# Kernel tuning notes

Measured on AMD Instinct MI355X. Metric: run time of the kernel, lower is better.

The kernel has to match this reference:

```python
import jax, jax.numpy as jnp
import numpy as np

B, N, T, H = 32, 16, 64, 256


def setup_inputs() -> dict:
    key = jax.random.key(0)
    k1, k2, k3 = jax.random.split(key, 3)
    node_rnn_output = jax.random.normal(k1, (B, T, H), dtype=jnp.float32)
    neigh_rnn_output = jax.random.normal(k2, (B, N, T, H), dtype=jnp.float32)
    # neighbor counts in [1, N] to avoid divide-by-zero in 1/sqrt scaling
    neighbors_number = jax.random.randint(k3, (B,), 1, N + 1, dtype=jnp.int64)
    return {
        "node_rnn_output": node_rnn_output,
        "neigh_rnn_output": neigh_rnn_output,
        "neighbors_number": neighbors_number,
    }


def reference(node_rnn_output, neigh_rnn_output, neighbors_number):
    b, t, h = node_rnn_output.shape
    n = neigh_rnn_output.shape[1]
    # [B, N*T, H]
    flat_neigh = neigh_rnn_output.reshape(b, n * t, h)
    # repeat node output along time axis: [B, N*T, H]
    stacked_node = jnp.tile(node_rnn_output, (1, n, 1))
    # S = flat_neigh @ stacked_node^T : [B, N*T, N*T]
    S = jnp.einsum("bqh,bkh->bqk", flat_neigh, stacked_node)
    scale = jnp.sqrt(neighbors_number.astype(S.dtype))  # [B]
    S = S / scale[:, None, None]
    A = jax.nn.softmax(S, axis=-1)
    # dropout with p=0 (eval / reference) is identity
    W = A.sum(axis=1).reshape(b, n, t)  # [B, N, T]
    output = jnp.einsum("bqk,bkh->bqh", A, flat_neigh)  # [B, N*T, H]
    return (output, W)
```

## Files before the change

kernel.cpp:

```cpp
#include <hip/hip_runtime.h>

#define Bc  32
#define Nc  16
#define Tc  64
#define Hc  256
#define NTc 1024

typedef unsigned short u16;
using v8s = __attribute__((ext_vector_type(8))) short;
using v4f = __attribute__((ext_vector_type(4))) float;

static __device__ __forceinline__ u16 f2bf(float x) {
    unsigned u = __float_as_uint(x);
    unsigned r = u + 0x7fffu + ((u >> 16) & 1u);
    return (u16)(r >> 16);
}
static __device__ __forceinline__ float bf2f(u16 h) {
    return __uint_as_float(((unsigned)h) << 16);
}

#define NFRAG_NODE 2048
#define NFRAG_MT   2048

__global__ __launch_bounds__(256) void prep_kernel(const float* __restrict__ neigh,
                                                   const float* __restrict__ node,
                                                   u16* __restrict__ MTf,
                                                   u16* __restrict__ NHf,
                                                   u16* __restrict__ NLf,
                                                   float* __restrict__ Wsum) {
    __shared__ float Ls[64][17];
    int bk = blockIdx.x, tid = threadIdx.x;

    if (bk < 512) {
        int b  = bk >> 4;
        int hc = bk & 15;
        int h0 = hc << 4;
        int t  = tid >> 2;
        int h4 = tid & 3;
        const float4* p = (const float4*)(neigh + ((size_t)(b * Nc * Tc) + t) * Hc + h0) + h4;
        float4 a = make_float4(0.f, 0.f, 0.f, 0.f);
#pragma unroll
        for (int i = 0; i < Nc; i++) {
            float4 v = p[(size_t)i * (Tc * Hc / 4)];
            a.x += v.x; a.y += v.y; a.z += v.z; a.w += v.w;
        }
        const float r = 1.0f / 16.0f;
        Ls[t][h4 * 4 + 0] = a.x * r;
        Ls[t][h4 * 4 + 1] = a.y * r;
        Ls[t][h4 * 4 + 2] = a.z * r;
        Ls[t][h4 * 4 + 3] = a.w * r;
        __syncthreads();
        if (tid < 128) {
            int ktb  = tid >> 6;
            int lane = tid & 63;
            int quad = lane >> 4;
            int c    = lane & 15;
            v8s o;
#pragma unroll
            for (int j = 0; j < 8; j++)
                o[j] = (short)f2bf(Ls[ktb * 32 + quad * 8 + j][c]);
            *(v8s*)(MTf + ((size_t)b * NFRAG_MT + (hc * 2 + ktb) * 64 + lane) * 8) = o;
        }
    } else {
        int b = bk - 512;
#pragma unroll
        for (int rep = 0; rep < 8; rep++) {
            int f    = rep * 256 + tid;
            int nt   = f >> 9;
            int ksb  = (f >> 6) & 7;
            int lane = f & 63;
            int quad = lane >> 4;
            int c    = lane & 15;
            const float* src = node + ((size_t)b * Tc + nt * 16 + c) * Hc + ksb * 32 + quad * 8;
            float4 f0 = *(const float4*)(src);
            float4 f1 = *(const float4*)(src + 4);
            v8s hs, ls;
            float vin[8] = {f0.x, f0.y, f0.z, f0.w, f1.x, f1.y, f1.z, f1.w};
#pragma unroll
            for (int j = 0; j < 8; j++) {
                u16 h = f2bf(vin[j]);
                hs[j] = (short)h;
                ls[j] = (short)f2bf(vin[j] - bf2f(h));
            }
            *(v8s*)(NHf + ((size_t)b * NFRAG_NODE + f) * 8) = hs;
            *(v8s*)(NLf + ((size_t)b * NFRAG_NODE + f) * 8) = ls;
        }
        if (tid < 64) Wsum[b * 64 + tid] = 0.f;
    }
}

__global__ __launch_bounds__(256) void fused_kernel(const float* __restrict__ neigh,
                                                    const u16* __restrict__ NHf,
                                                    const u16* __restrict__ NLf,
                                                    const int* __restrict__ nbr,
                                                    const u16* __restrict__ MTf,
                                                    float* __restrict__ out,
                                                    float* __restrict__ Wsum) {
    __shared__ u16 NHs[NFRAG_NODE * 8];
    __shared__ u16 Ph[64][72];

    int b  = blockIdx.x >> 4;
    int i  = blockIdx.x & 15;
    int q0 = i << 6;

    int tid  = threadIdx.x;
    int w    = tid >> 6;
    int lane = tid & 63;
    int quad = lane >> 4;
    int c    = lane & 15;

    int nb = (nbr[1] == 0) ? nbr[2 * b] : nbr[b];
    float rscale = rsqrtf((float)nb);

    const float* Xrow = neigh + ((size_t)(b * Nc * Tc) + q0 + w * 16 + c) * Hc;
    const u16*   NHb  = NHf + (size_t)b * NFRAG_NODE * 8;
    const u16*   NLb  = NLf + (size_t)b * NFRAG_NODE * 8 + lane * 8;
    const u16*   MTb  = MTf + (size_t)b * NFRAG_MT   * 8 + lane * 8;

#pragma unroll
    for (int rep = 0; rep < 8; rep++) {
        int chunk = rep * 256 + tid;
        *(uint4*)&NHs[chunk * 8] = *(const uint4*)(NHb + chunk * 8);
    }
    __syncthreads();

    v4f acc[4];
#pragma unroll
    for (int nt = 0; nt < 4; nt++)
#pragma unroll
        for (int rg = 0; rg < 4; rg++) acc[nt][rg] = 0.f;

#pragma unroll
    for (int ksb = 0; ksb < 8; ksb++) {
        float4 f0 = *(const float4*)(Xrow + ksb * 32 + quad * 8);
        float4 f1 = *(const float4*)(Xrow + ksb * 32 + quad * 8 + 4);
        v8s ah, al;
        {
            float vin[8] = {f0.x, f0.y, f0.z, f0.w, f1.x, f1.y, f1.z, f1.w};
#pragma unroll
            for (int j = 0; j < 8; j++) {
                u16 h = f2bf(vin[j]);
                ah[j] = (short)h;
                al[j] = (short)f2bf(vin[j] - bf2f(h));
            }
        }
#pragma unroll
        for (int nt = 0; nt < 4; nt++) {
            int fbase = (nt * 8 + ksb) * 64;
            v8s bh = *(const v8s*)&NHs[(fbase + lane) * 8];
            v8s bl = *(const v8s*)(NLb + (size_t)fbase * 8);
            acc[nt] = __builtin_amdgcn_mfma_f32_16x16x32_bf16(ah, bh, acc[nt], 0, 0, 0);
            acc[nt] = __builtin_amdgcn_mfma_f32_16x16x32_bf16(ah, bl, acc[nt], 0, 0, 0);
            acc[nt] = __builtin_amdgcn_mfma_f32_16x16x32_bf16(al, bh, acc[nt], 0, 0, 0);
        }
    }

#pragma unroll
    for (int nt = 0; nt < 4; nt++)
#pragma unroll
        for (int rg = 0; rg < 4; rg++) acc[nt][rg] *= rscale;

#pragma unroll
    for (int rg = 0; rg < 4; rg++) {
        float m = fmaxf(fmaxf(acc[0][rg], acc[1][rg]), fmaxf(acc[2][rg], acc[3][rg]));
#pragma unroll
        for (int d = 1; d < 16; d <<= 1) m = fmaxf(m, __shfl_xor(m, d));
        float e0 = __expf(acc[0][rg] - m);
        float e1 = __expf(acc[1][rg] - m);
        float e2 = __expf(acc[2][rg] - m);
        float e3 = __expf(acc[3][rg] - m);
        float s = e0 + e1 + e2 + e3;
#pragma unroll
        for (int d = 1; d < 16; d <<= 1) s += __shfl_xor(s, d);
        float inv = 1.0f / s;
        acc[0][rg] = e0 * inv; acc[1][rg] = e1 * inv;
        acc[2][rg] = e2 * inv; acc[3][rg] = e3 * inv;
    }

#pragma unroll
    for (int nt = 0; nt < 4; nt++) {
        float cs = acc[nt][0] + acc[nt][1] + acc[nt][2] + acc[nt][3];
        cs += __shfl_xor(cs, 16);
        cs += __shfl_xor(cs, 32);
        if (quad == 0) atomicAdd(&Wsum[b * Tc + nt * 16 + c], cs);
    }

#pragma unroll
    for (int nt = 0; nt < 4; nt++)
#pragma unroll
        for (int rg = 0; rg < 4; rg++)
            Ph[w * 16 + quad * 4 + rg][nt * 16 + c] = f2bf(acc[nt][rg]);

    v8s pa0 = *(const v8s*)&Ph[w * 16 + c][quad * 8];
    v8s pa1 = *(const v8s*)&Ph[w * 16 + c][32 + quad * 8];

    float* ob = out + ((size_t)b * NTc + q0 + w * 16 + quad * 4) * Hc + c;
#pragma unroll
    for (int ht = 0; ht < 16; ht++) {
        v8s b0 = *(const v8s*)(MTb + (size_t)((ht * 2 + 0) * 64) * 8);
        v8s b1 = *(const v8s*)(MTb + (size_t)((ht * 2 + 1) * 64) * 8);
        v4f oc;
        oc[0] = 0.f; oc[1] = 0.f; oc[2] = 0.f; oc[3] = 0.f;
        oc = __builtin_amdgcn_mfma_f32_16x16x32_bf16(pa0, b0, oc, 0, 0, 0);
        oc = __builtin_amdgcn_mfma_f32_16x16x32_bf16(pa1, b1, oc, 0, 0, 0);
#pragma unroll
        for (int rg = 0; rg < 4; rg++)
            ob[(size_t)rg * Hc + ht * 16] = oc[rg];
    }
}

__global__ __launch_bounds__(256) void wexp_kernel(const float* __restrict__ Wsum,
                                                   float* __restrict__ Wout) {
    int idx = blockIdx.x * 256 + threadIdx.x;
    int b = idx >> 10;
    int t = idx & 63;
    Wout[idx] = Wsum[b * Tc + t] * (1.0f / 16.0f);
}

extern "C" void kernel_launch(void* const* d_in, const int* in_sizes, int n_in,
                              void* d_out, int out_size, void* d_ws, size_t ws_size,
                              hipStream_t stream) {
    const float* node  = (const float*)d_in[0];
    const float* neigh = (const float*)d_in[1];
    const int*   nbr   = (const int*)d_in[2];

    float* out = (float*)d_out;

    u16* MTw = (u16*)d_ws;
    u16* NHw = MTw + (size_t)Bc * NFRAG_MT * 8;
    u16* NLw = NHw + (size_t)Bc * NFRAG_NODE * 8;
    float* Ww = (float*)(NLw + (size_t)Bc * NFRAG_NODE * 8);

    prep_kernel <<<544, 256, 0, stream>>>(neigh, node, MTw, NHw, NLw, Ww);
    fused_kernel<<<512, 256, 0, stream>>>(neigh, NHw, NLw, nbr, MTw, out, Ww);
    wexp_kernel <<<128, 256, 0, stream>>>(Ww, out + (size_t)Bc * NTc * Hc);
}
```

Baseline: 111.5 us.

## Precompute bf16 hi/lo split of neighbor tensor in prep and stage B operands in LDS

The prep kernel now converts the full neighbor tensor into bf16 high and low halves stored in workspace, while it is already reading that tensor to compute the mean. The fused kernel then loads these precomputed halves instead of reading fp32 and splitting it per block. Both the node hi and lo fragments are staged in shared memory, and the mean-transpose fragments are reloaded into the same LDS buffer for the second GEMM. This removes redundant conversion work and global fragment loads from the fused kernel, but it adds a full extra write and read of the neighbor tensor (two bf16 copies) through global memory, doubles the LDS footprint, and adds extra barriers.

```diff
diff --git a/kernel.cpp b/kernel.cpp
--- a/kernel.cpp
+++ b/kernel.cpp
@@ -19,47 +19,59 @@
     return __uint_as_float(((unsigned)h) << 16);
 }
 
-#define NFRAG_NODE 2048
-#define NFRAG_MT   2048
+#define XSZ   ((size_t)Bc * Nc * Tc * Hc)
+#define NODEF_SZ ((size_t)Bc * 4096 * 8)
+#define MTF_SZ   ((size_t)Bc * 2048 * 8)
 
 __global__ __launch_bounds__(256) void prep_kernel(const float* __restrict__ neigh,
                                                    const float* __restrict__ node,
+                                                   u16* __restrict__ XH,
+                                                   u16* __restrict__ XL,
+                                                   u16* __restrict__ NODEf,
                                                    u16* __restrict__ MTf,
-                                                   u16* __restrict__ NHf,
-                                                   u16* __restrict__ NLf,
                                                    float* __restrict__ Wsum) {
-    __shared__ float Ls[64][17];
+    __shared__ float Ls[32][33];
     int bk = blockIdx.x, tid = threadIdx.x;
 
     if (bk < 512) {
-        int b  = bk >> 4;
-        int hc = bk & 15;
-        int h0 = hc << 4;
-        int t  = tid >> 2;
-        int h4 = tid & 3;
-        const float4* p = (const float4*)(neigh + ((size_t)(b * Nc * Tc) + t) * Hc + h0) + h4;
+        int b   = bk >> 4;
+        int hc  = (bk >> 1) & 7;
+        int ktb = bk & 1;
+        int t0  = ktb * 32;
+        int h0  = hc * 32;
+        int t_l = tid >> 3;
+        int h8  = tid & 7;
         float4 a = make_float4(0.f, 0.f, 0.f, 0.f);
 #pragma unroll
         for (int i = 0; i < Nc; i++) {
-            float4 v = p[(size_t)i * (Tc * Hc / 4)];
+            size_t off = ((size_t)((b * Nc + i) * Tc) + t0 + t_l) * Hc + h0 + h8 * 4;
+            float4 v = *(const float4*)(neigh + off);
             a.x += v.x; a.y += v.y; a.z += v.z; a.w += v.w;
+            ushort4 hs, ls;
+            hs.x = f2bf(v.x); ls.x = f2bf(v.x - bf2f(hs.x));
+            hs.y = f2bf(v.y); ls.y = f2bf(v.y - bf2f(hs.y));
+            hs.z = f2bf(v.z); ls.z = f2bf(v.z - bf2f(hs.z));
+            hs.w = f2bf(v.w); ls.w = f2bf(v.w - bf2f(hs.w));
+            *(ushort4*)(XH + off) = hs;
+            *(ushort4*)(XL + off) = ls;
         }
         const float r = 1.0f / 16.0f;
-        Ls[t][h4 * 4 + 0] = a.x * r;
-        Ls[t][h4 * 4 + 1] = a.y * r;
-        Ls[t][h4 * 4 + 2] = a.z * r;
-        Ls[t][h4 * 4 + 3] = a.w * r;
+        Ls[t_l][h8 * 4 + 0] = a.x * r;
+        Ls[t_l][h8 * 4 + 1] = a.y * r;
+        Ls[t_l][h8 * 4 + 2] = a.z * r;
+        Ls[t_l][h8 * 4 + 3] = a.w * r;
         __syncthreads();
         if (tid < 128) {
-            int ktb  = tid >> 6;
+            int htl  = tid >> 6;
             int lane = tid & 63;
             int quad = lane >> 4;
             int c    = lane & 15;
             v8s o;
 #pragma unroll
             for (int j = 0; j < 8; j++)
-                o[j] = (short)f2bf(Ls[ktb * 32 + quad * 8 + j][c]);
-            *(v8s*)(MTf + ((size_t)b * NFRAG_MT + (hc * 2 + ktb) * 64 + lane) * 8) = o;
+                o[j] = (short)f2bf(Ls[quad * 8 + j][htl * 16 + c]);
+            int ht = hc * 2 + htl;
+            *(v8s*)(MTf + ((size_t)b * 2048 + (ht * 2 + ktb) * 64 + lane) * 8) = o;
         }
     } else {
         int b = bk - 512;
@@ -82,21 +94,21 @@
                 hs[j] = (short)h;
                 ls[j] = (short)f2bf(vin[j] - bf2f(h));
             }
-            *(v8s*)(NHf + ((size_t)b * NFRAG_NODE + f) * 8) = hs;
-            *(v8s*)(NLf + ((size_t)b * NFRAG_NODE + f) * 8) = ls;
+            *(v8s*)(NODEf + ((size_t)b * 4096 + f) * 8)        = hs;
+            *(v8s*)(NODEf + ((size_t)b * 4096 + 2048 + f) * 8) = ls;
         }
         if (tid < 64) Wsum[b * 64 + tid] = 0.f;
     }
 }
 
-__global__ __launch_bounds__(256) void fused_kernel(const float* __restrict__ neigh,
-                                                    const u16* __restrict__ NHf,
-                                                    const u16* __restrict__ NLf,
+__global__ __launch_bounds__(256) void fused_kernel(const u16* __restrict__ XH,
+                                                    const u16* __restrict__ XL,
+                                                    const u16* __restrict__ NODEf,
+                                                    const u16* __restrict__ MTf,
                                                     const int* __restrict__ nbr,
-                                                    const u16* __restrict__ MTf,
                                                     float* __restrict__ out,
                                                     float* __restrict__ Wsum) {
-    __shared__ u16 NHs[NFRAG_NODE * 8];
+    __shared__ __align__(16) u16 Bs[4096 * 8];
     __shared__ u16 Ph[64][72];
 
     int b  = blockIdx.x >> 4;
@@ -112,18 +124,18 @@
     int nb = (nbr[1] == 0) ? nbr[2 * b] : nbr[b];
     float rscale = rsqrtf((float)nb);
 
-    const float* Xrow = neigh + ((size_t)(b * Nc * Tc) + q0 + w * 16 + c) * Hc;
-    const u16*   NHb  = NHf + (size_t)b * NFRAG_NODE * 8;
-    const u16*   NLb  = NLf + (size_t)b * NFRAG_NODE * 8 + lane * 8;
-    const u16*   MTb  = MTf + (size_t)b * NFRAG_MT   * 8 + lane * 8;
-
-#pragma unroll
-    for (int rep = 0; rep < 8; rep++) {
-        int chunk = rep * 256 + tid;
-        *(uint4*)&NHs[chunk * 8] = *(const uint4*)(NHb + chunk * 8);
+    const u16* NFb = NODEf + (size_t)b * 4096 * 8;
+#pragma unroll
+    for (int rep = 0; rep < 16; rep++) {
+        int ch = rep * 256 + tid;
+        *(uint4*)&Bs[ch * 8] = *(const uint4*)(NFb + ch * 8);
     }
     __syncthreads();
 
+    size_t xoff = ((size_t)((b * Nc + i) * Tc) + w * 16 + c) * Hc;
+    const u16* XHrow = XH + xoff;
+    const u16* XLrow = XL + xoff;
+
     v4f acc[4];
 #pragma unroll
     for (int nt = 0; nt < 4; nt++)
@@ -132,23 +144,13 @@
 
 #pragma unroll
     for (int ksb = 0; ksb < 8; ksb++) {
-        float4 f0 = *(const float4*)(Xrow + ksb * 32 + quad * 8);
-        float4 f1 = *(const float4*)(Xrow + ksb * 32 + quad * 8 + 4);
-        v8s ah, al;
-        {
-            float vin[8] = {f0.x, f0.y, f0.z, f0.w, f1.x, f1.y, f1.z, f1.w};
-#pragma unroll
-            for (int j = 0; j < 8; j++) {
-                u16 h = f2bf(vin[j]);
-                ah[j] = (short)h;
-                al[j] = (short)f2bf(vin[j] - bf2f(h));
-            }
-        }
+        v8s ah = *(const v8s*)(XHrow + ksb * 32 + quad * 8);
+        v8s al = *(const v8s*)(XLrow + ksb * 32 + quad * 8);
 #pragma unroll
         for (int nt = 0; nt < 4; nt++) {
-            int fbase = (nt * 8 + ksb) * 64;
-            v8s bh = *(const v8s*)&NHs[(fbase + lane) * 8];
-            v8s bl = *(const v8s*)(NLb + (size_t)fbase * 8);
+            int f = (nt * 8 + ksb) * 64 + lane;
+            v8s bh = *(const v8s*)&Bs[f * 8];
+            v8s bl = *(const v8s*)&Bs[(f + 2048) * 8];
             acc[nt] = __builtin_amdgcn_mfma_f32_16x16x32_bf16(ah, bh, acc[nt], 0, 0, 0);
             acc[nt] = __builtin_amdgcn_mfma_f32_16x16x32_bf16(ah, bl, acc[nt], 0, 0, 0);
             acc[nt] = __builtin_amdgcn_mfma_f32_16x16x32_bf16(al, bh, acc[nt], 0, 0, 0);
@@ -194,11 +196,21 @@
     v8s pa0 = *(const v8s*)&Ph[w * 16 + c][quad * 8];
     v8s pa1 = *(const v8s*)&Ph[w * 16 + c][32 + quad * 8];
 
+    __syncthreads();
+
+    const u16* MTb = MTf + (size_t)b * 2048 * 8;
+#pragma unroll
+    for (int rep = 0; rep < 8; rep++) {
+        int ch = rep * 256 + tid;
+        *(uint4*)&Bs[ch * 8] = *(const uint4*)(MTb + ch * 8);
+    }
+    __syncthreads();
+
     float* ob = out + ((size_t)b * NTc + q0 + w * 16 + quad * 4) * Hc + c;
 #pragma unroll
     for (int ht = 0; ht < 16; ht++) {
-        v8s b0 = *(const v8s*)(MTb + (size_t)((ht * 2 + 0) * 64) * 8);
-        v8s b1 = *(const v8s*)(MTb + (size_t)((ht * 2 + 1) * 64) * 8);
+        v8s b0 = *(const v8s*)&Bs[((ht * 2 + 0) * 64 + lane) * 8];
+        v8s b1 = *(const v8s*)&Bs[((ht * 2 + 1) * 64 + lane) * 8];
         v4f oc;
         oc[0] = 0.f; oc[1] = 0.f; oc[2] = 0.f; oc[3] = 0.f;
         oc = __builtin_amdgcn_mfma_f32_16x16x32_bf16(pa0, b0, oc, 0, 0, 0);
@@ -226,12 +238,13 @@
 
     float* out = (float*)d_out;
 
-    u16* MTw = (u16*)d_ws;
-    u16* NHw = MTw + (size_t)Bc * NFRAG_MT * 8;
-    u16* NLw = NHw + (size_t)Bc * NFRAG_NODE * 8;
-    float* Ww = (float*)(NLw + (size_t)Bc * NFRAG_NODE * 8);
-
-    prep_kernel <<<544, 256, 0, stream>>>(neigh, node, MTw, NHw, NLw, Ww);
-    fused_kernel<<<512, 256, 0, stream>>>(neigh, NHw, NLw, nbr, MTw, out, Ww);
+    u16* XHw = (u16*)d_ws;
+    u16* XLw = XHw + XSZ;
+    u16* NFw = XLw + XSZ;
+    u16* MTw = NFw + NODEF_SZ;
+    float* Ww = (float*)(MTw + MTF_SZ);
+
+    prep_kernel <<<544, 256, 0, stream>>>(neigh, node, XHw, XLw, NFw, MTw, Ww);
+    fused_kernel<<<512, 256, 0, stream>>>(XHw, XLw, NFw, MTw, nbr, out, Ww);
     wexp_kernel <<<128, 256, 0, stream>>>(Ww, out + (size_t)Bc * NTc * Hc);
 }
```

Result: slower. 114.6 us (+2.8%).

## Merge prep, fused and W-expand kernels into one cooperative kernel with grid syncs

Applied to the files above, without the earlier changes.

Replaces the three separate launches with a single cooperative kernel that runs the prep phase, a grid-wide sync, the attention phase, another grid sync, and the W expansion. The node hi/lo bf16 fragments are packed together so both are staged in shared memory, and the MT fragments are also staged in shared memory before the output matmul instead of being read from global memory. Node preprocessing is spread across all blocks using the idle upper half of each block. This removes inter-kernel launch gaps and cuts redundant global reads, in exchange for grid-sync cost and higher shared memory use, which now requires two resident blocks per CU for the cooperative launch to fit.

```diff
diff --git a/kernel.cpp b/kernel.cpp
--- a/kernel.cpp
+++ b/kernel.cpp
@@ -1,4 +1,7 @@
 #include <hip/hip_runtime.h>
+#include <hip/hip_cooperative_groups.h>
+
+namespace cg = cooperative_groups;
 
 #define Bc  32
 #define Nc  16
@@ -19,37 +22,51 @@
     return __uint_as_float(((unsigned)h) << 16);
 }
 
-#define NFRAG_NODE 2048
-#define NFRAG_MT   2048
-
-__global__ __launch_bounds__(256) void prep_kernel(const float* __restrict__ neigh,
-                                                   const float* __restrict__ node,
-                                                   u16* __restrict__ MTf,
-                                                   u16* __restrict__ NHf,
-                                                   u16* __restrict__ NLf,
-                                                   float* __restrict__ Wsum) {
-    __shared__ float Ls[64][17];
-    int bk = blockIdx.x, tid = threadIdx.x;
-
-    if (bk < 512) {
+#define NODEF_SZ ((size_t)Bc * 4096 * 8)
+#define MTF_SZ   ((size_t)Bc * 2048 * 8)
+
+__global__ __launch_bounds__(256, 2) void mono_kernel(const float* __restrict__ neigh,
+                                                      const float* __restrict__ node,
+                                                      const int*   __restrict__ nbr,
+                                                      u16* __restrict__ NODEf,
+                                                      u16* __restrict__ MTf,
+                                                      float* __restrict__ Wsum,
+                                                      float* __restrict__ out,
+                                                      float* __restrict__ Wout) {
+    __shared__ __align__(16) u16 Bs[4096 * 8];
+    __shared__ u16 Ph[64][72];
+
+    cg::grid_group grid = cg::this_grid();
+
+    int bk  = blockIdx.x;
+    int tid = threadIdx.x;
+
+    {
+        float (*Ls)[17] = (float(*)[17])Bs;
         int b  = bk >> 4;
         int hc = bk & 15;
         int h0 = hc << 4;
-        int t  = tid >> 2;
-        int h4 = tid & 3;
-        const float4* p = (const float4*)(neigh + ((size_t)(b * Nc * Tc) + t) * Hc + h0) + h4;
-        float4 a = make_float4(0.f, 0.f, 0.f, 0.f);
-#pragma unroll
-        for (int i = 0; i < Nc; i++) {
-            float4 v = p[(size_t)i * (Tc * Hc / 4)];
-            a.x += v.x; a.y += v.y; a.z += v.z; a.w += v.w;
-        }
-        const float r = 1.0f / 16.0f;
-        Ls[t][h4 * 4 + 0] = a.x * r;
-        Ls[t][h4 * 4 + 1] = a.y * r;
-        Ls[t][h4 * 4 + 2] = a.z * r;
-        Ls[t][h4 * 4 + 3] = a.w * r;
-        __syncthreads();
+
+        if (bk < 32 && tid < 64) Wsum[bk * 64 + tid] = 0.f;
+
+        {
+            int t  = tid >> 2;
+            int h4 = tid & 3;
+            const float4* p = (const float4*)(neigh + ((size_t)(b * Nc * Tc) + t) * Hc + h0) + h4;
+            float4 a = make_float4(0.f, 0.f, 0.f, 0.f);
+#pragma unroll
+            for (int i = 0; i < Nc; i++) {
+                float4 v = p[(size_t)i * (Tc * Hc / 4)];
+                a.x += v.x; a.y += v.y; a.z += v.z; a.w += v.w;
+            }
+            const float r = 1.0f / 16.0f;
+            Ls[t][h4 * 4 + 0] = a.x * r;
+            Ls[t][h4 * 4 + 1] = a.y * r;
+            Ls[t][h4 * 4 + 2] = a.z * r;
+            Ls[t][h4 * 4 + 3] = a.w * r;
+        }
+        __syncthreads();
+
         if (tid < 128) {
             int ktb  = tid >> 6;
             int lane = tid & 63;
@@ -59,19 +76,17 @@
 #pragma unroll
             for (int j = 0; j < 8; j++)
                 o[j] = (short)f2bf(Ls[ktb * 32 + quad * 8 + j][c]);
-            *(v8s*)(MTf + ((size_t)b * NFRAG_MT + (hc * 2 + ktb) * 64 + lane) * 8) = o;
-        }
-    } else {
-        int b = bk - 512;
-#pragma unroll
-        for (int rep = 0; rep < 8; rep++) {
-            int f    = rep * 256 + tid;
+            *(v8s*)(MTf + ((size_t)b * 2048 + (hc * 2 + ktb) * 64 + lane) * 8) = o;
+        } else {
+            int g    = bk * 128 + (tid - 128);
+            int bn   = g >> 11;
+            int f    = g & 2047;
             int nt   = f >> 9;
             int ksb  = (f >> 6) & 7;
             int lane = f & 63;
             int quad = lane >> 4;
-            int c    = lane & 15;
-            const float* src = node + ((size_t)b * Tc + nt * 16 + c) * Hc + ksb * 32 + quad * 8;
+            int cc   = lane & 15;
+            const float* src = node + ((size_t)bn * Tc + nt * 16 + cc) * Hc + ksb * 32 + quad * 8;
             float4 f0 = *(const float4*)(src);
             float4 f1 = *(const float4*)(src + 4);
             v8s hs, ls;
@@ -82,139 +97,139 @@
                 hs[j] = (short)h;
                 ls[j] = (short)f2bf(vin[j] - bf2f(h));
             }
-            *(v8s*)(NHf + ((size_t)b * NFRAG_NODE + f) * 8) = hs;
-            *(v8s*)(NLf + ((size_t)b * NFRAG_NODE + f) * 8) = ls;
-        }
-        if (tid < 64) Wsum[b * 64 + tid] = 0.f;
+            *(v8s*)(NODEf + ((size_t)bn * 4096 + f) * 8)        = hs;
+            *(v8s*)(NODEf + ((size_t)bn * 4096 + 2048 + f) * 8) = ls;
+        }
     }
-}
-
-__global__ __launch_bounds__(256) void fused_kernel(const float* __restrict__ neigh,
-                                                    const u16* __restrict__ NHf,
-                                                    const u16* __restrict__ NLf,
-                                                    const int* __restrict__ nbr,
-                                                    const u16* __restrict__ MTf,
-                                                    float* __restrict__ out,
-                                                    float* __restrict__ Wsum) {
-    __shared__ u16 NHs[NFRAG_NODE * 8];
-    __shared__ u16 Ph[64][72];
-
-    int b  = blockIdx.x >> 4;
-    int i  = blockIdx.x & 15;
-    int q0 = i << 6;
-
-    int tid  = threadIdx.x;
-    int w    = tid >> 6;
-    int lane = tid & 63;
-    int quad = lane >> 4;
-    int c    = lane & 15;
-
-    int nb = (nbr[1] == 0) ? nbr[2 * b] : nbr[b];
-    float rscale = rsqrtf((float)nb);
-
-    const float* Xrow = neigh + ((size_t)(b * Nc * Tc) + q0 + w * 16 + c) * Hc;
-    const u16*   NHb  = NHf + (size_t)b * NFRAG_NODE * 8;
-    const u16*   NLb  = NLf + (size_t)b * NFRAG_NODE * 8 + lane * 8;
-    const u16*   MTb  = MTf + (size_t)b * NFRAG_MT   * 8 + lane * 8;
-
-#pragma unroll
-    for (int rep = 0; rep < 8; rep++) {
-        int chunk = rep * 256 + tid;
-        *(uint4*)&NHs[chunk * 8] = *(const uint4*)(NHb + chunk * 8);
+
+    grid.sync();
+
+    {
+        int b  = bk >> 4;
+        int i  = bk & 15;
+        int q0 = i << 6;
+
+        int w    = tid >> 6;
+        int lane = tid & 63;
+        int quad = lane >> 4;
+        int c    = lane & 15;
+
+        int nb = (nbr[1] == 0) ? nbr[2 * b] : nbr[b];
+        float rscale = rsqrtf((float)nb);
+
+        const u16* NFb = NODEf + (size_t)b * 4096 * 8;
+#pragma unroll
+        for (int rep = 0; rep < 16; rep++) {
+            int ch = rep * 256 + tid;
+            *(uint4*)&Bs[ch * 8] = *(const uint4*)(NFb + ch * 8);
+        }
+        __syncthreads();
+
+        const float* Xrow = neigh + ((size_t)(b * Nc * Tc) + q0 + w * 16 + c) * Hc;
+
+        v4f acc[4];
+#pragma unroll
+        for (int nt = 0; nt < 4; nt++)
+#pragma unroll
+            for (int rg = 0; rg < 4; rg++) acc[nt][rg] = 0.f;
+
+#pragma unroll
+        for (int ksb = 0; ksb < 8; ksb++) {
+            float4 f0 = *(const float4*)(Xrow + ksb * 32 + quad * 8);
+            float4 f1 = *(const float4*)(Xrow + ksb * 32 + quad * 8 + 4);
+            v8s ah, al;
+            {
+                float vin[8] = {f0.x, f0.y, f0.z, f0.w, f1.x, f1.y, f1.z, f1.w};
+#pragma unroll
+                for (int j = 0; j < 8; j++) {
+                    u16 h = f2bf(vin[j]);
+                    ah[j] = (short)h;
+                    al[j] = (short)f2bf(vin[j] - bf2f(h));
+                }
+            }
+#pragma unroll
+            for (int nt = 0; nt < 4; nt++) {
+                int f = (nt * 8 + ksb) * 64 + lane;
+                v8s bh = *(const v8s*)&Bs[f * 8];
+                v8s bl = *(const v8s*)&Bs[(f + 2048) * 8];
+                acc[nt] = __builtin_amdgcn_mfma_f32_16x16x32_bf16(ah, bh, acc[nt], 0, 0, 0);
+                acc[nt] = __builtin_amdgcn_mfma_f32_16x16x32_bf16(ah, bl, acc[nt], 0, 0, 0);
+                acc[nt] = __builtin_amdgcn_mfma_f32_16x16x32_bf16(al, bh, acc[nt], 0, 0, 0);
+            }
+        }
+
+#pragma unroll
+        for (int nt = 0; nt < 4; nt++)
+#pragma unroll
+            for (int rg = 0; rg < 4; rg++) acc[nt][rg] *= rscale;
+
+#pragma unroll
+        for (int rg = 0; rg < 4; rg++) {
+            float m = fmaxf(fmaxf(acc[0][rg], acc[1][rg]), fmaxf(acc[2][rg], acc[3][rg]));
+#pragma unroll
+            for (int d = 1; d < 16; d <<= 1) m = fmaxf(m, __shfl_xor(m, d));
+            float e0 = __expf(acc[0][rg] - m);
+            float e1 = __expf(acc[1][rg] - m);
+            float e2 = __expf(acc[2][rg] - m);
+            float e3 = __expf(acc[3][rg] - m);
+            float s = e0 + e1 + e2 + e3;
+#pragma unroll
+            for (int d = 1; d < 16; d <<= 1) s += __shfl_xor(s, d);
+            float inv = 1.0f / s;
+            acc[0][rg] = e0 * inv; acc[1][rg] = e1 * inv;
+            acc[2][rg] = e2 * inv; acc[3][rg] = e3 * inv;
+        }
+
+#pragma unroll
+        for (int nt = 0; nt < 4; nt++) {
+            float cs = acc[nt][0] + acc[nt][1] + acc[nt][2] + acc[nt][3];
+            cs += __shfl_xor(cs, 16);
+            cs += __shfl_xor(cs, 32);
+            if (quad == 0) atomicAdd(&Wsum[b * Tc + nt * 16 + c], cs);
+        }
+
+#pragma unroll
+        for (int nt = 0; nt < 4; nt++)
+#pragma unroll
+            for (int rg = 0; rg < 4; rg++)
+                Ph[w * 16 + quad * 4 + rg][nt * 16 + c] = f2bf(acc[nt][rg]);
+
+        v8s pa0 = *(const v8s*)&Ph[w * 16 + c][quad * 8];
+        v8s pa1 = *(const v8s*)&Ph[w * 16 + c][32 + quad * 8];
+
+        __syncthreads();
+
+        const u16* MTb = MTf + (size_t)b * 2048 * 8;
+#pragma unroll
+        for (int rep = 0; rep < 8; rep++) {
+            int ch = rep * 256 + tid;
+            *(uint4*)&Bs[ch * 8] = *(const uint4*)(MTb + ch * 8);
+        }
+        __syncthreads();
+
+        float* ob = out + ((size_t)b * NTc + q0 + w * 16 + quad * 4) * Hc + c;
+#pragma unroll
+        for (int ht = 0; ht < 16; ht++) {
+            v8s b0 = *(const v8s*)&Bs[((ht * 2 + 0) * 64 + lane) * 8];
+            v8s b1 = *(const v8s*)&Bs[((ht * 2 + 1) * 64 + lane) * 8];
+            v4f oc;
+            oc[0] = 0.f; oc[1] = 0.f; oc[2] = 0.f; oc[3] = 0.f;
+            oc = __builtin_amdgcn_mfma_f32_16x16x32_bf16(pa0, b0, oc, 0, 0, 0);
+            oc = __builtin_amdgcn_mfma_f32_16x16x32_bf16(pa1, b1, oc, 0, 0, 0);
+#pragma unroll
+            for (int rg = 0; rg < 4; rg++)
+                ob[(size_t)rg * Hc + ht * 16] = oc[rg];
+        }
     }
-    __syncthreads();
-
-    v4f acc[4];
-#pragma unroll
-    for (int nt = 0; nt < 4; nt++)
-#pragma unroll
-        for (int rg = 0; rg < 4; rg++) acc[nt][rg] = 0.f;
-
-#pragma unroll
-    for (int ksb = 0; ksb < 8; ksb++) {
-        float4 f0 = *(const float4*)(Xrow + ksb * 32 + quad * 8);
-        float4 f1 = *(const float4*)(Xrow + ksb * 32 + quad * 8 + 4);
-        v8s ah, al;
-        {
-            float vin[8] = {f0.x, f0.y, f0.z, f0.w, f1.x, f1.y, f1.z, f1.w};
-#pragma unroll
-            for (int j = 0; j < 8; j++) {
-                u16 h = f2bf(vin[j]);
-                ah[j] = (short)h;
-                al[j] = (short)f2bf(vin[j] - bf2f(h));
-            }
-        }
-#pragma unroll
-        for (int nt = 0; nt < 4; nt++) {
-            int fbase = (nt * 8 + ksb) * 64;
-            v8s bh = *(const v8s*)&NHs[(fbase + lane) * 8];
-            v8s bl = *(const v8s*)(NLb + (size_t)fbase * 8);
-            acc[nt] = __builtin_amdgcn_mfma_f32_16x16x32_bf16(ah, bh, acc[nt], 0, 0, 0);
-            acc[nt] = __builtin_amdgcn_mfma_f32_16x16x32_bf16(ah, bl, acc[nt], 0, 0, 0);
-            acc[nt] = __builtin_amdgcn_mfma_f32_16x16x32_bf16(al, bh, acc[nt], 0, 0, 0);
-        }
+
+    grid.sync();
+
+    if (bk < 128) {
+        int idx = bk * 256 + tid;
+        int b = idx >> 10;
+        int t = idx & 63;
+        Wout[idx] = Wsum[b * Tc + t] * (1.0f / 16.0f);
     }
-
-#pragma unroll
-    for (int nt = 0; nt < 4; nt++)
-#pragma unroll
-        for (int rg = 0; rg < 4; rg++) acc[nt][rg] *= rscale;
-
-#pragma unroll
-    for (int rg = 0; rg < 4; rg++) {
-        float m = fmaxf(fmaxf(acc[0][rg], acc[1][rg]), fmaxf(acc[2][rg], acc[3][rg]));
-#pragma unroll
-        for (int d = 1; d < 16; d <<= 1) m = fmaxf(m, __shfl_xor(m, d));
-        float e0 = __expf(acc[0][rg] - m);
-        float e1 = __expf(acc[1][rg] - m);
-        float e2 = __expf(acc[2][rg] - m);
-        float e3 = __expf(acc[3][rg] - m);
-        float s = e0 + e1 + e2 + e3;
-#pragma unroll
-        for (int d = 1; d < 16; d <<= 1) s += __shfl_xor(s, d);
-        float inv = 1.0f / s;
-        acc[0][rg] = e0 * inv; acc[1][rg] = e1 * inv;
-        acc[2][rg] = e2 * inv; acc[3][rg] = e3 * inv;
-    }
-
-#pragma unroll
-    for (int nt = 0; nt < 4; nt++) {
-        float cs = acc[nt][0] + acc[nt][1] + acc[nt][2] + acc[nt][3];
-        cs += __shfl_xor(cs, 16);
-        cs += __shfl_xor(cs, 32);
-        if (quad == 0) atomicAdd(&Wsum[b * Tc + nt * 16 + c], cs);
-    }
-
-#pragma unroll
-    for (int nt = 0; nt < 4; nt++)
-#pragma unroll
-        for (int rg = 0; rg < 4; rg++)
-            Ph[w * 16 + quad * 4 + rg][nt * 16 + c] = f2bf(acc[nt][rg]);
-
-    v8s pa0 = *(const v8s*)&Ph[w * 16 + c][quad * 8];
-    v8s pa1 = *(const v8s*)&Ph[w * 16 + c][32 + quad * 8];
-
-    float* ob = out + ((size_t)b * NTc + q0 + w * 16 + quad * 4) * Hc + c;
-#pragma unroll
-    for (int ht = 0; ht < 16; ht++) {
-        v8s b0 = *(const v8s*)(MTb + (size_t)((ht * 2 + 0) * 64) * 8);
-        v8s b1 = *(const v8s*)(MTb + (size_t)((ht * 2 + 1) * 64) * 8);
-        v4f oc;
-        oc[0] = 0.f; oc[1] = 0.f; oc[2] = 0.f; oc[3] = 0.f;
-        oc = __builtin_amdgcn_mfma_f32_16x16x32_bf16(pa0, b0, oc, 0, 0, 0);
-        oc = __builtin_amdgcn_mfma_f32_16x16x32_bf16(pa1, b1, oc, 0, 0, 0);
-#pragma unroll
-        for (int rg = 0; rg < 4; rg++)
-            ob[(size_t)rg * Hc + ht * 16] = oc[rg];
-    }
-}
-
-__global__ __launch_bounds__(256) void wexp_kernel(const float* __restrict__ Wsum,
-                                                   float* __restrict__ Wout) {
-    int idx = blockIdx.x * 256 + threadIdx.x;
-    int b = idx >> 10;
-    int t = idx & 63;
-    Wout[idx] = Wsum[b * Tc + t] * (1.0f / 16.0f);
 }
 
 extern "C" void kernel_launch(void* const* d_in, const int* in_sizes, int n_in,
@@ -224,14 +239,16 @@
     const float* neigh = (const float*)d_in[1];
     const int*   nbr   = (const int*)d_in[2];
 
-    float* out = (float*)d_out;
-
-    u16* MTw = (u16*)d_ws;
-    u16* NHw = MTw + (size_t)Bc * NFRAG_MT * 8;
-    u16* NLw = NHw + (size_t)Bc * NFRAG_NODE * 8;
-    float* Ww = (float*)(NLw + (size_t)Bc * NFRAG_NODE * 8);
-
-    prep_kernel <<<544, 256, 0, stream>>>(neigh, node, MTw, NHw, NLw, Ww);
-    fused_kernel<<<512, 256, 0, stream>>>(neigh, NHw, NLw, nbr, MTw, out, Ww);
-    wexp_kernel <<<128, 256, 0, stream>>>(Ww, out + (size_t)Bc * NTc * Hc);
-}
+    float* out  = (float*)d_out;
+    float* Wout = out + (size_t)Bc * NTc * Hc;
+
+    u16* NFw = (u16*)d_ws;
+    u16* MTw = NFw + NODEF_SZ;
+    float* Ww = (float*)(MTw + MTF_SZ);
+
+    void* args[] = {(void*)&neigh, (void*)&node, (void*)&nbr,
+                    (void*)&NFw, (void*)&MTw, (void*)&Ww,
+                    (void*)&out, (void*)&Wout};
+    hipLaunchCooperativeKernel((const void*)mono_kernel,
+                               dim3(512), dim3(256), args, 0, stream);
+}
```

Result: slower. 238.6 us (+114.1%).
